# Kernel tuning notes

Hardware: AMD Instinct MI355X
Metric: run time of the kernel (lower is better)

The kernel has to match this reference:

```python
import jax, jax.numpy as jnp
import numpy as np

C = 256
NUM_HEADS = 8
NUM_GROUPS = 32
EPS = 1e-5


def setup_inputs() -> dict:
    key = jax.random.key(0)
    ks = jax.random.split(key, 7)
    B, H, W = 2, 64, 64
    x = jax.random.normal(ks[0], (B, C, H, W), dtype=jnp.float32)
    norm_gamma = jnp.ones((C,), dtype=jnp.float32)
    norm_beta = jnp.zeros((C,), dtype=jnp.float32)
    # 1x1 convs == per-pixel linear layers; store weights as (out_ch, in_ch)
    qkv_w = jax.random.normal(ks[1], (3 * C, C), dtype=jnp.float32) * (1.0 / np.sqrt(C))
    qkv_b = jnp.zeros((3 * C,), dtype=jnp.float32)
    proj_w = jax.random.normal(ks[2], (C, C), dtype=jnp.float32) * (1.0 / np.sqrt(C))
    proj_b = jnp.zeros((C,), dtype=jnp.float32)
    return {"x": x, "norm_gamma": norm_gamma, "norm_beta": norm_beta,
            "qkv_w": qkv_w, "qkv_b": qkv_b, "proj_w": proj_w, "proj_b": proj_b}


def _group_norm(x, gamma, beta):
    B, Cc, H, W = x.shape
    xg = x.reshape(B, NUM_GROUPS, Cc // NUM_GROUPS, H, W)
    mean = xg.mean(axis=(2, 3, 4), keepdims=True)
    var = xg.var(axis=(2, 3, 4), keepdims=True)
    xn = ((xg - mean) * jax.lax.rsqrt(var + EPS)).reshape(B, Cc, H, W)
    return xn * gamma[None, :, None, None] + beta[None, :, None, None]


def reference(x, norm_gamma, norm_beta, qkv_w, qkv_b, proj_w, proj_b):
    B, Cc, H, W = x.shape
    hd = Cc // NUM_HEADS
    N = H * W

    h = _group_norm(x, norm_gamma, norm_beta)
    # 1x1 conv: (3C,C) x (B,C,H,W) -> (B,3C,H,W)
    qkv = jnp.einsum('oc,bchw->bohw', qkv_w, h) + qkv_b[None, :, None, None]
    q, k, v = jnp.split(qkv, 3, axis=1)

    def heads(t):  # (B,C,H,W) -> (B,heads,N,hd)
        return t.reshape(B, NUM_HEADS, hd, N).transpose(0, 1, 3, 2)

    q, k, v = heads(q), heads(k), heads(v)
    scale = hd ** (-0.5)
    attn = jax.nn.softmax(jnp.einsum('bhnd,bhmd->bhnm', q, k) * scale, axis=-1)
    out = jnp.einsum('bhnm,bhmd->bhnd', attn, v)  # (B,heads,N,hd)
    out = out.transpose(0, 1, 3, 2).reshape(B, Cc, H, W)
    out = jnp.einsum('oc,bchw->bohw', proj_w, out) + proj_b[None, :, None, None]
    return x + out
```

## Files before the change

### kernel.cpp

```cpp
#include <hip/hip_runtime.h>
#include <math.h>

#define C_    256
#define NH    8
#define HD_   32
#define NG    32
#define CPG   8
#define NPIX  4096
#define BATCH 2
#define EPSV  1e-5f
#define SLOG2 0.25503489f
#define MF    16.0f
#define KVB   64
#define LSTR  72
#define KPS2  2048

typedef __bf16 bf16x8 __attribute__((ext_vector_type(8)));
typedef __bf16 bf16x4 __attribute__((ext_vector_type(4)));
typedef float  f32x4  __attribute__((ext_vector_type(4)));

__global__ __launch_bounds__(256) void gn_stats_kernel(const float* __restrict__ x,
                                                       float* __restrict__ stats) {
    const int blk = blockIdx.x;
    const int b = blk >> 5, g = blk & 31;
    const float* __restrict__ xp = x + ((size_t)(b * C_ + g * CPG)) * NPIX;

    float s = 0.f, ss = 0.f;
    for (int i = threadIdx.x * 4; i < CPG * NPIX; i += 256 * 4) {
        const float4 v = *(const float4*)(xp + i);
        s  += v.x + v.y + v.z + v.w;
        ss += v.x * v.x + v.y * v.y + v.z * v.z + v.w * v.w;
    }
    #pragma unroll
    for (int off = 32; off; off >>= 1) {
        s  += __shfl_down(s, off);
        ss += __shfl_down(ss, off);
    }
    __shared__ float ls[4], lss[4];
    const int wid = threadIdx.x >> 6, lane = threadIdx.x & 63;
    if (lane == 0) { ls[wid] = s; lss[wid] = ss; }
    __syncthreads();
    if (threadIdx.x == 0) {
        float S = 0.f, SS = 0.f;
        #pragma unroll
        for (int w = 0; w < 4; ++w) { S += ls[w]; SS += lss[w]; }
        const float inv_n = 1.0f / (float)(CPG * NPIX);
        const float mean = S * inv_n;
        const float var  = SS * inv_n - mean * mean;
        stats[blk * 2 + 0] = mean;
        stats[blk * 2 + 1] = rsqrtf(var + EPSV);
    }
}

__global__ __launch_bounds__(256) void wconv_kernel(const float* __restrict__ qw,
                                                    const float* __restrict__ pw,
                                                    __bf16* __restrict__ wbq,
                                                    __bf16* __restrict__ wbp) {
    const int i = (blockIdx.x * 256 + threadIdx.x) * 4;
    const float* src;
    __bf16* dst;
    int off;
    if (i < 768 * 256) { src = qw; dst = wbq; off = i; }
    else { src = pw; dst = wbp; off = i - 768 * 256; }
    const float4 v = *(const float4*)(src + off);
    bf16x4 o;
    o[0] = (__bf16)v.x; o[1] = (__bf16)v.y; o[2] = (__bf16)v.z; o[3] = (__bf16)v.w;
    *(bf16x4*)(dst + off) = o;
}

__global__ __launch_bounds__(256) void ht_kernel(const float* __restrict__ x,
                                                 const float* __restrict__ stats,
                                                 const float* __restrict__ gamma,
                                                 const float* __restrict__ beta,
                                                 __bf16* __restrict__ Ht) {
    const int b = blockIdx.y;
    const int n0 = blockIdx.x * 64;
    __shared__ __align__(16) __bf16 tile[64][264];
    const int nn = (threadIdx.x & 15) * 4;
    #pragma unroll
    for (int p = 0; p < 16; ++p) {
        const int c = (threadIdx.x >> 4) + p * 16;
        const float4 v = *(const float4*)(x + ((size_t)(b * C_ + c)) * NPIX + n0 + nn);
        const int g = c >> 3;
        const float mean = stats[(b * NG + g) * 2 + 0];
        const float rstd = stats[(b * NG + g) * 2 + 1];
        const float ga = gamma[c] * rstd;
        const float be = beta[c] - mean * ga;
        tile[nn + 0][c] = (__bf16)(v.x * ga + be);
        tile[nn + 1][c] = (__bf16)(v.y * ga + be);
        tile[nn + 2][c] = (__bf16)(v.z * ga + be);
        tile[nn + 3][c] = (__bf16)(v.w * ga + be);
    }
    __syncthreads();
    #pragma unroll
    for (int p = 0; p < 8; ++p) {
        const int id = p * 256 + threadIdx.x;
        const int row = id >> 5;
        const int ch  = id & 31;
        *(bf16x8*)(Ht + ((size_t)(b * NPIX) + n0 + row) * C_ + ch * 8) =
            *(const bf16x8*)(&tile[row][ch * 8]);
    }
}

__global__ __launch_bounds__(256) void qkv_gemm_kernel(const __bf16* __restrict__ wbq,
                                                       const float* __restrict__ bias,
                                                       const __bf16* __restrict__ Ht,
                                                       __bf16* __restrict__ Qb,
                                                       __bf16* __restrict__ Kb,
                                                       __bf16* __restrict__ Vb) {
    const int b = blockIdx.z;
    const int n0 = blockIdx.x * 32;
    const int wave = threadIdx.x >> 6, lane = threadIdx.x & 63;
    const int col = lane & 15, g = lane >> 4;
    const int m0 = blockIdx.y * 256 + wave * 64;
    const __bf16* __restrict__ hp = Ht + (size_t)b * NPIX * C_;

    f32x4 acc[4][2];
    #pragma unroll
    for (int i = 0; i < 4; ++i)
        #pragma unroll
        for (int j = 0; j < 2; ++j) acc[i][j] = (f32x4){0.f, 0.f, 0.f, 0.f};

    #pragma unroll
    for (int c0 = 0; c0 < C_; c0 += 32) {
        bf16x8 la[4], lb[2];
        #pragma unroll
        for (int mb = 0; mb < 4; ++mb)
            la[mb] = *(const bf16x8*)(wbq + (size_t)(m0 + mb * 16 + col) * C_ + c0 + g * 8);
        #pragma unroll
        for (int nb = 0; nb < 2; ++nb)
            lb[nb] = *(const bf16x8*)(hp + (size_t)(n0 + nb * 16 + col) * C_ + c0 + g * 8);
        #pragma unroll
        for (int mb = 0; mb < 4; ++mb)
            #pragma unroll
            for (int nb = 0; nb < 2; ++nb)
                acc[mb][nb] = __builtin_amdgcn_mfma_f32_16x16x32_bf16(la[mb], lb[nb], acc[mb][nb], 0, 0, 0);
    }

    #pragma unroll
    for (int mb = 0; mb < 4; ++mb) {
        const int mbase = m0 + mb * 16 + 4 * g;
        const float4 b4 = *(const float4*)(bias + mbase);
        const int route = mbase >> 8;
        const int bh = b * NH + ((mbase >> 5) & 7);
        const int d0 = mbase & 31;
        #pragma unroll
        for (int nb = 0; nb < 2; ++nb) {
            const int n = n0 + nb * 16 + col;
            f32x4 v = acc[mb][nb];
            v[0] += b4.x; v[1] += b4.y; v[2] += b4.z; v[3] += b4.w;
            if (route == 0) {
                bf16x4 o;
                #pragma unroll
                for (int r = 0; r < 4; ++r) o[r] = (__bf16)(v[r] * SLOG2);
                *(bf16x4*)(Qb + (((size_t)bh * NPIX + n) << 5) + d0) = o;
            } else if (route == 1) {
                bf16x4 o;
                #pragma unroll
                for (int r = 0; r < 4; ++r) o[r] = (__bf16)v[r];
                *(bf16x4*)(Kb + (((size_t)bh * NPIX + n) << 5) + d0) = o;
            } else {
                #pragma unroll
                for (int r = 0; r < 4; ++r)
                    Vb[((size_t)bh * HD_ + d0 + r) * NPIX + n] = (__bf16)v[r];
            }
        }
    }
}

__global__ __launch_bounds__(512) void attn_kernel(const __bf16* __restrict__ Qb,
                                                   const __bf16* __restrict__ Kb,
                                                   const __bf16* __restrict__ Vb,
                                                   __bf16* __restrict__ aot) {
    __shared__ __align__(16) char smem[55296];
    __bf16 (*Ks)[2][KVB][LSTR] = (__bf16 (*)[2][KVB][LSTR])(smem);
    __bf16 (*Vs)[2][HD_][LSTR] = (__bf16 (*)[2][HD_][LSTR])(smem + 36864);
    float* pbuf = (float*)smem;

    const int b = blockIdx.z, h = blockIdx.y;
    const int wave = threadIdx.x >> 6, lane = threadIdx.x & 63;
    const int hw = wave >> 2, wv = wave & 3;
    const int col = lane & 15, g = lane >> 4;
    const int bh = b * NH + h;
    const int q0 = blockIdx.x * 128 + wv * 32;

    const __bf16* __restrict__ qp = Qb + ((size_t)bh * NPIX + q0) * HD_;
    const __bf16* __restrict__ kp = Kb + ((size_t)bh * NPIX + hw * KPS2) * HD_;
    const __bf16* __restrict__ vp = Vb + (size_t)bh * HD_ * NPIX + hw * KPS2;

    const int sk_key = wv * 16 + (lane >> 2);
    const int sk_seg = (lane & 3) * 8;
    const int sv_d   = wv * 8 + (lane >> 3);
    const int sv_seg = (lane & 7) * 8;
    const __bf16* __restrict__ kg = kp + (size_t)sk_key * HD_ + sk_seg;
    const __bf16* __restrict__ vg = vp + (size_t)sv_d * NPIX + sv_seg;

    const bf16x8 fq0 = *(const bf16x8*)(qp + col * HD_ + g * 8);
    const bf16x8 fq1 = *(const bf16x8*)(qp + (16 + col) * HD_ + g * 8);

    bf16x8 ones;
    #pragma unroll
    for (int j = 0; j < 8; ++j) ones[j] = (__bf16)1.0f;
    const f32x4 mfc = {-MF, -MF, -MF, -MF};

    f32x4 acc00 = {0.f,0.f,0.f,0.f}, acc01 = {0.f,0.f,0.f,0.f};
    f32x4 acc10 = {0.f,0.f,0.f,0.f}, acc11 = {0.f,0.f,0.f,0.f};
    f32x4 accL0 = {0.f,0.f,0.f,0.f}, accL1 = {0.f,0.f,0.f,0.f};

    {
        const bf16x8 rk = *(const bf16x8*)(kg);
        const bf16x8 rv = *(const bf16x8*)(vg);
        *(bf16x8*)&Ks[hw][0][sk_key][sk_seg] = rk;
        *(bf16x8*)&Vs[hw][0][sv_d][sv_seg] = rv;
    }
    __syncthreads();

    const int nt = KPS2 / KVB;
    for (int t = 0; t < nt; ++t) {
        const int cur = t & 1;
        bf16x8 nk, nv;
        const bool more = (t + 1 < nt);
        {
            const size_t koff = (size_t)(more ? (t + 1) * KVB : 0);
            nk = *(const bf16x8*)(kg + koff * HD_);
            nv = *(const bf16x8*)(vg + koff);
        }

        #pragma unroll
        for (int kk = 0; kk < KVB; kk += 32) {
            const bf16x8 fk0 = *(const bf16x8*)(&Ks[hw][cur][kk + col][g * 8]);
            const bf16x8 fk1 = *(const bf16x8*)(&Ks[hw][cur][kk + 16 + col][g * 8]);
            const bf16x4 va0 = *(const bf16x4*)(&Vs[hw][cur][col][kk + 4 * g]);
            const bf16x4 va1 = *(const bf16x4*)(&Vs[hw][cur][col][kk + 16 + 4 * g]);
            const bf16x4 vb0 = *(const bf16x4*)(&Vs[hw][cur][col + 16][kk + 4 * g]);
            const bf16x4 vb1 = *(const bf16x4*)(&Vs[hw][cur][col + 16][kk + 16 + 4 * g]);

            __builtin_amdgcn_s_setprio(1);
            f32x4 s00 = __builtin_amdgcn_mfma_f32_16x16x32_bf16(fk0, fq0, mfc, 0, 0, 0);
            f32x4 s10 = __builtin_amdgcn_mfma_f32_16x16x32_bf16(fk1, fq0, mfc, 0, 0, 0);
            f32x4 s01 = __builtin_amdgcn_mfma_f32_16x16x32_bf16(fk0, fq1, mfc, 0, 0, 0);
            f32x4 s11 = __builtin_amdgcn_mfma_f32_16x16x32_bf16(fk1, fq1, mfc, 0, 0, 0);
            __builtin_amdgcn_s_setprio(0);

            float p0[8], p1[8];
            #pragma unroll
            for (int r = 0; r < 4; ++r) {
                p0[r]     = __builtin_amdgcn_exp2f(s00[r]);
                p0[4 + r] = __builtin_amdgcn_exp2f(s10[r]);
                p1[r]     = __builtin_amdgcn_exp2f(s01[r]);
                p1[4 + r] = __builtin_amdgcn_exp2f(s11[r]);
            }

            bf16x8 fp0, fp1, fv0, fv1;
            #pragma unroll
            for (int j = 0; j < 8; ++j) { fp0[j] = (__bf16)p0[j]; fp1[j] = (__bf16)p1[j]; }
            #pragma unroll
            for (int j = 0; j < 4; ++j) {
                fv0[j] = va0[j]; fv0[4 + j] = va1[j];
                fv1[j] = vb0[j]; fv1[4 + j] = vb1[j];
            }

            __builtin_amdgcn_s_setprio(1);
            accL0 = __builtin_amdgcn_mfma_f32_16x16x32_bf16(ones, fp0, accL0, 0, 0, 0);
            accL1 = __builtin_amdgcn_mfma_f32_16x16x32_bf16(ones, fp1, accL1, 0, 0, 0);
            acc00 = __builtin_amdgcn_mfma_f32_16x16x32_bf16(fv0, fp0, acc00, 0, 0, 0);
            acc01 = __builtin_amdgcn_mfma_f32_16x16x32_bf16(fv1, fp0, acc01, 0, 0, 0);
            acc10 = __builtin_amdgcn_mfma_f32_16x16x32_bf16(fv0, fp1, acc10, 0, 0, 0);
            acc11 = __builtin_amdgcn_mfma_f32_16x16x32_bf16(fv1, fp1, acc11, 0, 0, 0);
            __builtin_amdgcn_s_setprio(0);
        }

        if (more) {
            *(bf16x8*)&Ks[hw][cur ^ 1][sk_key][sk_seg] = nk;
            *(bf16x8*)&Vs[hw][cur ^ 1][sv_d][sv_seg] = nv;
        }
        __syncthreads();
    }

    float l0 = accL0[0], l1 = accL1[0];

    if (hw == 1) {
        float* pp = pbuf + ((size_t)wv * 64 + lane) * 20;
        *(f32x4*)(pp + 0)  = acc00;
        *(f32x4*)(pp + 4)  = acc01;
        *(f32x4*)(pp + 8)  = acc10;
        *(f32x4*)(pp + 12) = acc11;
        pp[16] = l0; pp[17] = l1;
    }
    __syncthreads();
    if (hw == 0) {
        const float* pp = pbuf + ((size_t)wv * 64 + lane) * 20;
        const f32x4 b00 = *(const f32x4*)(pp + 0);
        const f32x4 b01 = *(const f32x4*)(pp + 4);
        const f32x4 b10 = *(const f32x4*)(pp + 8);
        const f32x4 b11 = *(const f32x4*)(pp + 12);
        #pragma unroll
        for (int r = 0; r < 4; ++r) {
            acc00[r] += b00[r]; acc01[r] += b01[r];
            acc10[r] += b10[r]; acc11[r] += b11[r];
        }
        const float inv0 = 1.0f / (l0 + pp[16]);
        const float inv1 = 1.0f / (l1 + pp[17]);
        const int cb = h * HD_ + 4 * g;
        {
            __bf16* op = aot + ((size_t)(b * NPIX) + q0 + col) * C_ + cb;
            bf16x4 o0, o1;
            #pragma unroll
            for (int r = 0; r < 4; ++r) { o0[r] = (__bf16)(acc00[r] * inv0); o1[r] = (__bf16)(acc01[r] * inv0); }
            *(bf16x4*)(op) = o0;
            *(bf16x4*)(op + 16) = o1;
        }
        {
            __bf16* op = aot + ((size_t)(b * NPIX) + q0 + 16 + col) * C_ + cb;
            bf16x4 o0, o1;
            #pragma unroll
            for (int r = 0; r < 4; ++r) { o0[r] = (__bf16)(acc10[r] * inv1); o1[r] = (__bf16)(acc11[r] * inv1); }
            *(bf16x4*)(op) = o0;
            *(bf16x4*)(op + 16) = o1;
        }
    }
}

__global__ __launch_bounds__(256) void proj_gemm_kernel(const __bf16* __restrict__ wbp,
                                                        const float* __restrict__ bias,
                                                        const __bf16* __restrict__ aot,
                                                        const float* __restrict__ x,
                                                        float* __restrict__ out) {
    const int b = blockIdx.z;
    const int wave = threadIdx.x >> 6, lane = threadIdx.x & 63;
    const int col = lane & 15, g = lane >> 4;
    const int n0 = blockIdx.x * 64 + (wave & 1) * 32;
    const int m0 = blockIdx.y * 64 + (wave >> 1) * 32;
    const __bf16* __restrict__ ap = aot + (size_t)b * NPIX * C_;

    f32x4 acc[2][2];
    #pragma unroll
    for (int i = 0; i < 2; ++i)
        #pragma unroll
        for (int j = 0; j < 2; ++j) acc[i][j] = (f32x4){0.f, 0.f, 0.f, 0.f};

    #pragma unroll
    for (int c0 = 0; c0 < C_; c0 += 32) {
        bf16x8 la[2], lb[2];
        #pragma unroll
        for (int mb = 0; mb < 2; ++mb)
            la[mb] = *(const bf16x8*)(wbp + (size_t)(m0 + mb * 16 + col) * C_ + c0 + g * 8);
        #pragma unroll
        for (int nb = 0; nb < 2; ++nb)
            lb[nb] = *(const bf16x8*)(ap + (size_t)(n0 + nb * 16 + col) * C_ + c0 + g * 8);
        #pragma unroll
        for (int mb = 0; mb < 2; ++mb)
            #pragma unroll
            for (int nb = 0; nb < 2; ++nb)
                acc[mb][nb] = __builtin_amdgcn_mfma_f32_16x16x32_bf16(la[mb], lb[nb], acc[mb][nb], 0, 0, 0);
    }

    #pragma unroll
    for (int mb = 0; mb < 2; ++mb) {
        const int mbase = m0 + mb * 16 + 4 * g;
        const float4 b4 = *(const float4*)(bias + mbase);
        const float bias_r[4] = {b4.x, b4.y, b4.z, b4.w};
        #pragma unroll
        for (int nb = 0; nb < 2; ++nb) {
            const int n = n0 + nb * 16 + col;
            #pragma unroll
            for (int r = 0; r < 4; ++r) {
                const size_t idx = ((size_t)(b * C_ + mbase + r)) * NPIX + n;
                out[idx] = acc[mb][nb][r] + bias_r[r] + x[idx];
            }
        }
    }
}

extern "C" void kernel_launch(void* const* d_in, const int* in_sizes, int n_in,
                              void* d_out, int out_size, void* d_ws, size_t ws_size,
                              hipStream_t stream) {
    (void)in_sizes; (void)n_in; (void)out_size; (void)ws_size;
    const float* x      = (const float*)d_in[0];
    const float* gamma  = (const float*)d_in[1];
    const float* beta   = (const float*)d_in[2];
    const float* qkv_w  = (const float*)d_in[3];
    const float* qkv_b  = (const float*)d_in[4];
    const float* proj_w = (const float*)d_in[5];
    const float* proj_b = (const float*)d_in[6];
    float* out = (float*)d_out;

    char* ws = (char*)d_ws;
    __bf16* wbq  = (__bf16*)(ws);
    __bf16* wbp  = (__bf16*)(ws + 0x60000);
    float*  stats= (float*) (ws + 0x80000);
    __bf16* Ht   = (__bf16*)(ws + 0x100000);
    __bf16* Qb   = (__bf16*)(ws + 0x500000);
    __bf16* Kb   = (__bf16*)(ws + 0x900000);
    __bf16* Vb   = (__bf16*)(ws + 0xD00000);
    __bf16* aot  = (__bf16*)(ws + 0x1100000);

    gn_stats_kernel<<<dim3(BATCH * NG), dim3(256), 0, stream>>>(x, stats);
    wconv_kernel<<<dim3(256), dim3(256), 0, stream>>>(qkv_w, proj_w, wbq, wbp);
    ht_kernel<<<dim3(NPIX / 64, BATCH), dim3(256), 0, stream>>>(x, stats, gamma, beta, Ht);
    qkv_gemm_kernel<<<dim3(NPIX / 32, 3, BATCH), dim3(256), 0, stream>>>(wbq, qkv_b, Ht, Qb, Kb, Vb);
    attn_kernel<<<dim3(NPIX / 128, NH, BATCH), dim3(512), 0, stream>>>(Qb, Kb, Vb, aot);
    proj_gemm_kernel<<<dim3(NPIX / 64, C_ / 64, BATCH), dim3(256), 0, stream>>>(wbp, proj_b, aot, x, out);
}
```

Before: 96.54 us.

## Fuse prep kernels, shrink K LDS stride, permute V layout for 8-wide loads

Merges the group-norm stats and weight conversion kernels into one launch to save a kernel launch. In the attention kernel, the K tile stride drops from 72 to 40 and V is stored in LDS with a permuted column order. This lets each lane read a contiguous bf16x8 V fragment instead of four bf16x4 loads plus register shuffling. Shared memory per block shrinks, and launch bounds request higher occupancy. The tradeoff is split V stores and possible new bank conflicts from the changed strides.

```diff
diff --git a/kernel.cpp b/kernel.cpp
--- a/kernel.cpp
+++ b/kernel.cpp
@@ -12,15 +12,33 @@
 #define SLOG2 0.25503489f
 #define MF    16.0f
 #define KVB   64
-#define LSTR  72
+#define KSTR  40
+#define VSTR  72
 #define KPS2  2048
 
 typedef __bf16 bf16x8 __attribute__((ext_vector_type(8)));
 typedef __bf16 bf16x4 __attribute__((ext_vector_type(4)));
 typedef float  f32x4  __attribute__((ext_vector_type(4)));
 
-__global__ __launch_bounds__(256) void gn_stats_kernel(const float* __restrict__ x,
-                                                       float* __restrict__ stats) {
+__global__ __launch_bounds__(256) void prep_kernel(const float* __restrict__ x,
+                                                   float* __restrict__ stats,
+                                                   const float* __restrict__ qw,
+                                                   const float* __restrict__ pw,
+                                                   __bf16* __restrict__ wbq,
+                                                   __bf16* __restrict__ wbp) {
+    if (blockIdx.x >= 64) {
+        const int i = ((blockIdx.x - 64) * 256 + threadIdx.x) * 4;
+        const float* src;
+        __bf16* dst;
+        int off;
+        if (i < 768 * 256) { src = qw; dst = wbq; off = i; }
+        else { src = pw; dst = wbp; off = i - 768 * 256; }
+        const float4 v = *(const float4*)(src + off);
+        bf16x4 o;
+        o[0] = (__bf16)v.x; o[1] = (__bf16)v.y; o[2] = (__bf16)v.z; o[3] = (__bf16)v.w;
+        *(bf16x4*)(dst + off) = o;
+        return;
+    }
     const int blk = blockIdx.x;
     const int b = blk >> 5, g = blk & 31;
     const float* __restrict__ xp = x + ((size_t)(b * C_ + g * CPG)) * NPIX;
@@ -50,22 +68,6 @@
         stats[blk * 2 + 0] = mean;
         stats[blk * 2 + 1] = rsqrtf(var + EPSV);
     }
-}
-
-__global__ __launch_bounds__(256) void wconv_kernel(const float* __restrict__ qw,
-                                                    const float* __restrict__ pw,
-                                                    __bf16* __restrict__ wbq,
-                                                    __bf16* __restrict__ wbp) {
-    const int i = (blockIdx.x * 256 + threadIdx.x) * 4;
-    const float* src;
-    __bf16* dst;
-    int off;
-    if (i < 768 * 256) { src = qw; dst = wbq; off = i; }
-    else { src = pw; dst = wbp; off = i - 768 * 256; }
-    const float4 v = *(const float4*)(src + off);
-    bf16x4 o;
-    o[0] = (__bf16)v.x; o[1] = (__bf16)v.y; o[2] = (__bf16)v.z; o[3] = (__bf16)v.w;
-    *(bf16x4*)(dst + off) = o;
 }
 
 __global__ __launch_bounds__(256) void ht_kernel(const float* __restrict__ x,
@@ -168,13 +170,13 @@
     }
 }
 
-__global__ __launch_bounds__(512) void attn_kernel(const __bf16* __restrict__ Qb,
-                                                   const __bf16* __restrict__ Kb,
-                                                   const __bf16* __restrict__ Vb,
-                                                   __bf16* __restrict__ aot) {
-    __shared__ __align__(16) char smem[55296];
-    __bf16 (*Ks)[2][KVB][LSTR] = (__bf16 (*)[2][KVB][LSTR])(smem);
-    __bf16 (*Vs)[2][HD_][LSTR] = (__bf16 (*)[2][HD_][LSTR])(smem + 36864);
+__global__ __launch_bounds__(512, 8) void attn_kernel(const __bf16* __restrict__ Qb,
+                                                      const __bf16* __restrict__ Kb,
+                                                      const __bf16* __restrict__ Vb,
+                                                      __bf16* __restrict__ aot) {
+    __shared__ __align__(16) char smem[38912];
+    __bf16 (*Ks)[2][KVB][KSTR] = (__bf16 (*)[2][KVB][KSTR])(smem);
+    __bf16 (*Vs)[2][HD_][VSTR] = (__bf16 (*)[2][HD_][VSTR])(smem + 20480);
     float* pbuf = (float*)smem;
 
     const int b = blockIdx.z, h = blockIdx.y;
@@ -192,6 +194,7 @@
     const int sk_seg = (lane & 3) * 8;
     const int sv_d   = wv * 8 + (lane >> 3);
     const int sv_seg = (lane & 7) * 8;
+    const int vslot  = (sv_seg & 32) + ((((sv_seg & 15) >> 2) << 3)) + (((sv_seg >> 4) & 1) << 2);
     const __bf16* __restrict__ kg = kp + (size_t)sk_key * HD_ + sk_seg;
     const __bf16* __restrict__ vg = vp + (size_t)sv_d * NPIX + sv_seg;
 
@@ -211,7 +214,11 @@
         const bf16x8 rk = *(const bf16x8*)(kg);
         const bf16x8 rv = *(const bf16x8*)(vg);
         *(bf16x8*)&Ks[hw][0][sk_key][sk_seg] = rk;
-        *(bf16x8*)&Vs[hw][0][sv_d][sv_seg] = rv;
+        bf16x4 lo, hi;
+        #pragma unroll
+        for (int j = 0; j < 4; ++j) { lo[j] = rv[j]; hi[j] = rv[4 + j]; }
+        *(bf16x4*)&Vs[hw][0][sv_d][vslot]     = lo;
+        *(bf16x4*)&Vs[hw][0][sv_d][vslot + 8] = hi;
     }
     __syncthreads();
 
@@ -230,10 +237,8 @@
         for (int kk = 0; kk < KVB; kk += 32) {
             const bf16x8 fk0 = *(const bf16x8*)(&Ks[hw][cur][kk + col][g * 8]);
             const bf16x8 fk1 = *(const bf16x8*)(&Ks[hw][cur][kk + 16 + col][g * 8]);
-            const bf16x4 va0 = *(const bf16x4*)(&Vs[hw][cur][col][kk + 4 * g]);
-            const bf16x4 va1 = *(const bf16x4*)(&Vs[hw][cur][col][kk + 16 + 4 * g]);
-            const bf16x4 vb0 = *(const bf16x4*)(&Vs[hw][cur][col + 16][kk + 4 * g]);
-            const bf16x4 vb1 = *(const bf16x4*)(&Vs[hw][cur][col + 16][kk + 16 + 4 * g]);
+            const bf16x8 fv0 = *(const bf16x8*)(&Vs[hw][cur][col][kk + 8 * g]);
+            const bf16x8 fv1 = *(const bf16x8*)(&Vs[hw][cur][col + 16][kk + 8 * g]);
 
             __builtin_amdgcn_s_setprio(1);
             f32x4 s00 = __builtin_amdgcn_mfma_f32_16x16x32_bf16(fk0, fq0, mfc, 0, 0, 0);
@@ -251,14 +256,9 @@
                 p1[4 + r] = __builtin_amdgcn_exp2f(s11[r]);
             }
 
-            bf16x8 fp0, fp1, fv0, fv1;
+            bf16x8 fp0, fp1;
             #pragma unroll
             for (int j = 0; j < 8; ++j) { fp0[j] = (__bf16)p0[j]; fp1[j] = (__bf16)p1[j]; }
-            #pragma unroll
-            for (int j = 0; j < 4; ++j) {
-                fv0[j] = va0[j]; fv0[4 + j] = va1[j];
-                fv1[j] = vb0[j]; fv1[4 + j] = vb1[j];
-            }
 
             __builtin_amdgcn_s_setprio(1);
             accL0 = __builtin_amdgcn_mfma_f32_16x16x32_bf16(ones, fp0, accL0, 0, 0, 0);
@@ -272,7 +272,11 @@
 
         if (more) {
             *(bf16x8*)&Ks[hw][cur ^ 1][sk_key][sk_seg] = nk;
-            *(bf16x8*)&Vs[hw][cur ^ 1][sv_d][sv_seg] = nv;
+            bf16x4 lo, hi;
+            #pragma unroll
+            for (int j = 0; j < 4; ++j) { lo[j] = nv[j]; hi[j] = nv[4 + j]; }
+            *(bf16x4*)&Vs[hw][cur ^ 1][sv_d][vslot]     = lo;
+            *(bf16x4*)&Vs[hw][cur ^ 1][sv_d][vslot + 8] = hi;
         }
         __syncthreads();
     }
@@ -395,8 +399,7 @@
     __bf16* Vb   = (__bf16*)(ws + 0xD00000);
     __bf16* aot  = (__bf16*)(ws + 0x1100000);
 
-    gn_stats_kernel<<<dim3(BATCH * NG), dim3(256), 0, stream>>>(x, stats);
-    wconv_kernel<<<dim3(256), dim3(256), 0, stream>>>(qkv_w, proj_w, wbq, wbp);
+    prep_kernel<<<dim3(320), dim3(256), 0, stream>>>(x, stats, qkv_w, proj_w, wbq, wbp);
     ht_kernel<<<dim3(NPIX / 64, BATCH), dim3(256), 0, stream>>>(x, stats, gamma, beta, Ht);
     qkv_gemm_kernel<<<dim3(NPIX / 32, 3, BATCH), dim3(256), 0, stream>>>(wbq, qkv_b, Ht, Qb, Kb, Vb);
     attn_kernel<<<dim3(NPIX / 128, NH, BATCH), dim3(512), 0, stream>>>(Qb, Kb, Vb, aot);
```

New measurement: 288.6 us. 199% more time.
